# Optimization experiments

Measured on AMD Instinct MI355X. Metric: run time of the kernel, lower is better.

The kernel has to match this reference:

```python
import jax, jax.numpy as jnp
import numpy as np

B, S, F, H = 64, 512, 512, 1024


def setup_inputs() -> dict:
    key = jax.random.key(0)
    ks = jax.random.split(key, 12)
    s_in = 1.0 / np.sqrt(H)
    return {
        "x": jax.random.normal(ks[0], (B, S, F), dtype=jnp.float32),
        "W_ih0": jax.random.uniform(ks[1], (H, F), jnp.float32, -s_in, s_in),
        "W_hh0": jax.random.uniform(ks[2], (H, H), jnp.float32, -s_in, s_in),
        "b_ih0": jax.random.uniform(ks[3], (H,), jnp.float32, -s_in, s_in),
        "b_hh0": jax.random.uniform(ks[4], (H,), jnp.float32, -s_in, s_in),
        "W_ih1": jax.random.uniform(ks[5], (H, H), jnp.float32, -s_in, s_in),
        "W_hh1": jax.random.uniform(ks[6], (H, H), jnp.float32, -s_in, s_in),
        "b_ih1": jax.random.uniform(ks[7], (H,), jnp.float32, -s_in, s_in),
        "b_hh1": jax.random.uniform(ks[8], (H,), jnp.float32, -s_in, s_in),
        "fc_w": jax.random.uniform(ks[9], (1, H), jnp.float32, -s_in, s_in),
        "fc_b": jax.random.uniform(ks[10], (1,), jnp.float32, -s_in, s_in),
    }


def _rnn_layer(x_seq, W_ih, W_hh, b_ih, b_hh):
    # x_seq: [B, S, Fin]; PyTorch RNN step: h_t = tanh(x W_ih^T + b_ih + h W_hh^T + b_hh)
    x_proj = jnp.einsum("bsf,hf->bsh", x_seq, W_ih) + b_ih + b_hh  # precompute input part
    h0 = jnp.zeros((x_seq.shape[0], W_hh.shape[0]), x_seq.dtype)

    def step(h, xp):
        h_new = jnp.tanh(xp + h @ W_hh.T)
        return h_new, h_new

    _, ys = jax.lax.scan(step, h0, jnp.swapaxes(x_proj, 0, 1))  # [S, B, H]
    return jnp.swapaxes(ys, 0, 1)  # [B, S, H]


def reference(x, W_ih0, W_hh0, b_ih0, b_hh0, W_ih1, W_hh1, b_ih1, b_hh1, fc_w, fc_b):
    h1 = _rnn_layer(x, W_ih0, W_hh0, b_ih0, b_hh0)
    h2 = _rnn_layer(h1, W_ih1, W_hh1, b_ih1, b_hh1)
    last = h2[:, -1, :]  # [B, H]
    logits = (last @ fc_w.T + fc_b).squeeze(-1)  # [B]
    return jax.nn.sigmoid(logits)
```

## Files before the change

### kernel.cpp

```cpp
#include <hip/hip_runtime.h>

typedef unsigned short u16;
typedef __attribute__((ext_vector_type(8))) short short8;
typedef __attribute__((ext_vector_type(4))) float f32x4;

#define GLP(p) ((const __attribute__((address_space(1))) void*)(p))
#define LDSP(p) ((__attribute__((address_space(3))) void*)(p))

__device__ inline u16 f2bf(float f) {
  unsigned u = __float_as_uint(f);
  return (u16)((u + 0x7fffu + ((u >> 16) & 1u)) >> 16);
}
__device__ inline float bf2f(u16 h) {
  return __uint_as_float(((unsigned)h) << 16);
}
__device__ inline float tanh_fast(float x) {
  float e = __expf(2.0f * x);
  return 1.0f - 2.0f / (e + 1.0f);
}

__device__ inline void store_short_sc(u16* p, unsigned v) {
  asm volatile("global_store_short %0, %1, off sc0 sc1" :: "v"(p), "v"(v) : "memory");
}
__device__ inline void store_int_sc(int* p, int v) {
  asm volatile("global_store_dword %0, %1, off sc0 sc1" :: "v"(p), "v"(v) : "memory");
}
__device__ inline int load_int_sc(const int* p) {
  int v;
  asm volatile("global_load_dword %0, %1, off sc0 sc1\n\t"
               "s_waitcnt vmcnt(0)"
               : "=&v"(v) : "v"(p) : "memory");
  return v;
}
__device__ inline void load8_sc(const u16* plo, const u16* phi,
                                short8& d0, short8& d1, short8& d2, short8& d3,
                                short8& d4, short8& d5, short8& d6, short8& d7) {
  asm volatile(
      "global_load_dwordx4 %0, %8, off sc0 sc1\n\t"
      "global_load_dwordx4 %1, %8, off offset:1024 sc0 sc1\n\t"
      "global_load_dwordx4 %2, %8, off offset:2048 sc0 sc1\n\t"
      "global_load_dwordx4 %3, %8, off offset:3072 sc0 sc1\n\t"
      "global_load_dwordx4 %4, %9, off sc0 sc1\n\t"
      "global_load_dwordx4 %5, %9, off offset:1024 sc0 sc1\n\t"
      "global_load_dwordx4 %6, %9, off offset:2048 sc0 sc1\n\t"
      "global_load_dwordx4 %7, %9, off offset:3072 sc0 sc1\n\t"
      : "=&v"(d0), "=&v"(d1), "=&v"(d2), "=&v"(d3),
        "=&v"(d4), "=&v"(d5), "=&v"(d6), "=&v"(d7)
      : "v"(plo), "v"(phi)
      : "memory");
}
__device__ inline void wait_all16(short8& a0, short8& a1, short8& a2, short8& a3,
                                  short8& a4, short8& a5, short8& a6, short8& a7,
                                  short8& b0, short8& b1, short8& b2, short8& b3,
                                  short8& b4, short8& b5, short8& b6, short8& b7) {
  asm volatile("s_waitcnt vmcnt(0)"
               : "+v"(a0), "+v"(a1), "+v"(a2), "+v"(a3),
                 "+v"(a4), "+v"(a5), "+v"(a6), "+v"(a7),
                 "+v"(b0), "+v"(b1), "+v"(b2), "+v"(b3),
                 "+v"(b4), "+v"(b5), "+v"(b6), "+v"(b7)
               :: "memory");
}
__device__ inline void poll_flags(const int* fbase, int lane, int target) {
  const int* fp = fbase + lane * 32;
  while (load_int_sc(fp) < target) {}
}

__device__ inline void convseg(const float* __restrict__ s, u16* __restrict__ d,
                               long n4, long t, long S) {
  for (long i = t; i < n4; i += S) {
    float4 v = ((const float4*)s)[i];
    ushort4 o;
    o.x = f2bf(v.x); o.y = f2bf(v.y); o.z = f2bf(v.z); o.w = f2bf(v.w);
    ((ushort4*)d)[i] = o;
  }
}

__global__ __launch_bounds__(256) void prep_kernel(
    const float* __restrict__ x, const float* __restrict__ wih0,
    const float* __restrict__ whh0, const float* __restrict__ wih1,
    const float* __restrict__ whh1,
    u16* __restrict__ xb, u16* __restrict__ wih0b, u16* __restrict__ whh0b,
    u16* __restrict__ wih1b, u16* __restrict__ whh1b,
    u16* __restrict__ hbufs, int* __restrict__ bar) {
  long t = blockIdx.x * 256L + threadIdx.x;
  long S = (long)gridDim.x * 256L;
  convseg(x,    xb,    16777216 / 4, t, S);
  convseg(wih0, wih0b,   524288 / 4, t, S);
  convseg(whh0, whh0b,  1048576 / 4, t, S);
  convseg(wih1, wih1b,  1048576 / 4, t, S);
  convseg(whh1, whh1b,  1048576 / 4, t, S);
  ushort4 z4 = make_ushort4(0, 0, 0, 0);
  for (long i = t; i < 65536; i += S) ((ushort4*)hbufs)[i] = z4;
  int4 zi = make_int4(0, 0, 0, 0);
  for (long i = t; i < 4096; i += S) ((int4*)bar)[i] = zi;
}

__global__ __launch_bounds__(256, 2) void gemm_xproj(
    const u16* __restrict__ A,
    const u16* __restrict__ Bw,
    const float* __restrict__ bi, const float* __restrict__ bh,
    u16* __restrict__ C) {
  __shared__ u16 As[128 * 64];
  __shared__ u16 Bs[128 * 64];
  const int tid = threadIdx.x;
  const int lane = tid & 63;
  const int w = tid >> 6;
  const int ln = lane & 15, kg = lane >> 4;
  const int m0 = blockIdx.x * 128;
  const int n0 = blockIdx.y * 128;
  const int mi = (w & 1) * 64, ni = (w >> 1) * 64;

  f32x4 acc[4][4] = {};
  float bias[4];
#pragma unroll
  for (int nj = 0; nj < 4; ++nj) bias[nj] = bi[n0 + ni + nj * 16 + ln] + bh[n0 + ni + nj * 16 + ln];

  const int lrow = lane >> 3;
  const int lcol = (lane & 7) * 8;

  for (int kt = 0; kt < 512; kt += 64) {
#pragma unroll
    for (int i = 0; i < 4; ++i) {
      int row = i * 32 + w * 8;
      const u16* ga = A + (long)(m0 + row + lrow) * 512 + kt + lcol;
      __builtin_amdgcn_global_load_lds(GLP(ga), LDSP(As + row * 64), 16, 0, 0);
      const u16* gb = Bw + (long)(n0 + row + lrow) * 512 + kt + lcol;
      __builtin_amdgcn_global_load_lds(GLP(gb), LDSP(Bs + row * 64), 16, 0, 0);
    }
    __syncthreads();
#pragma unroll
    for (int kc = 0; kc < 64; kc += 32) {
      short8 af[4], bf[4];
#pragma unroll
      for (int i = 0; i < 4; ++i) {
        af[i] = *(const short8*)(As + (mi + i * 16 + ln) * 64 + kc + kg * 8);
        bf[i] = *(const short8*)(Bs + (ni + i * 16 + ln) * 64 + kc + kg * 8);
      }
#pragma unroll
      for (int a = 0; a < 4; ++a)
#pragma unroll
        for (int b = 0; b < 4; ++b)
          acc[a][b] = __builtin_amdgcn_mfma_f32_16x16x32_bf16(af[a], bf[b], acc[a][b], 0, 0, 0);
    }
    __syncthreads();
  }
#pragma unroll
  for (int a = 0; a < 4; ++a)
#pragma unroll
    for (int b = 0; b < 4; ++b)
#pragma unroll
      for (int r = 0; r < 4; ++r) {
        int m = m0 + mi + a * 16 + kg * 4 + r;
        int n = n0 + ni + b * 16 + ln;
        C[(long)m * 1024 + n] = f2bf(acc[a][b][r] + bias[b]);
      }
}

__global__ __launch_bounds__(256, 1) void rnn_persist(
    const u16* __restrict__ whh0, const u16* __restrict__ wih1,
    const u16* __restrict__ whh1, const u16* __restrict__ xp0,
    const float* __restrict__ bih1, const float* __restrict__ bhh1,
    u16* __restrict__ h1buf, u16* __restrict__ h2buf, int* __restrict__ bar) {
  const int tid = threadIdx.x;
  const int lane = tid & 63;
  const int w = tid >> 6;
  const int ln = lane & 15, kg = lane >> 4;
  const int q = blockIdx.x >> 6;
  const int c = blockIdx.x & 63;
  const int m0 = q * 16;
  const int j0 = c * 16;
  const int kb = w * 256;

  short8 WA[8], W1[8], W2[8];
#pragma unroll
  for (int i = 0; i < 8; ++i) {
    int off = (j0 + ln) * 1024 + kb + i * 32 + kg * 8;
    WA[i] = *(const short8*)(whh0 + off);
    W1[i] = *(const short8*)(wih1 + off);
    W2[i] = *(const short8*)(whh1 + off);
  }
  const float bias1 = bih1[j0 + ln] + bhh1[j0 + ln];

  __shared__ float red[2][2][4][256];
  int* flags = bar + q * 64 * 32;
  int* myF = flags + c * 32;

  const int lbase = (w * 16 + (kg >> 1)) * 256 + ln * 16 + (kg & 1) * 8;
  const u16* hq1 = h1buf + q * 16384 + lbase;
  const u16* hq2 = h2buf + q * 16384 + lbase;

  short8 H1[8], H2[8];
  u16 xpv[4];

  short8 zz = {0, 0, 0, 0, 0, 0, 0, 0};
#pragma unroll
  for (int i = 0; i < 8; ++i) { H1[i] = zz; H2[i] = zz; }
  if (w == 0) {
#pragma unroll
    for (int r = 0; r < 4; ++r)
      xpv[r] = xp0[((long)(m0 + kg * 4 + r) * 512 + 0) * 1024 + j0 + ln];
  }

  for (int it = 0; it <= 512; ++it) {
    const int rp = it & 1;
    f32x4 accA = {}, accB = {};
#pragma unroll
    for (int i = 0; i < 8; ++i) accA = __builtin_amdgcn_mfma_f32_16x16x32_bf16(H1[i], WA[i], accA, 0, 0, 0);
#pragma unroll
    for (int i = 0; i < 8; ++i) accB = __builtin_amdgcn_mfma_f32_16x16x32_bf16(H1[i], W1[i], accB, 0, 0, 0);
#pragma unroll
    for (int i = 0; i < 8; ++i) accB = __builtin_amdgcn_mfma_f32_16x16x32_bf16(H2[i], W2[i], accB, 0, 0, 0);
    *(f32x4*)&red[rp][0][w][lane * 4] = accA;
    *(f32x4*)&red[rp][1][w][lane * 4] = accB;
    __syncthreads();

    if (w == 0) {
      if (it < 512) {
        f32x4 s = *(const f32x4*)&red[rp][0][0][lane * 4];
        s += *(const f32x4*)&red[rp][0][1][lane * 4];
        s += *(const f32x4*)&red[rp][0][2][lane * 4];
        s += *(const f32x4*)&red[rp][0][3][lane * 4];
        u16* h1w = h1buf + (it & 1) * 65536 + q * 16384 + c * 256;
#pragma unroll
        for (int r = 0; r < 4; ++r) {
          float z = s[r] + bf2f(xpv[r]);
          store_short_sc(h1w + (kg * 4 + r) * 16 + ln, (unsigned)f2bf(tanh_fast(z)));
        }
        asm volatile("s_waitcnt vmcnt(0)" ::: "memory");
      }
    } else if (w == 1) {
      if (it >= 1) {
        f32x4 s = *(const f32x4*)&red[rp][1][0][lane * 4];
        s += *(const f32x4*)&red[rp][1][1][lane * 4];
        s += *(const f32x4*)&red[rp][1][2][lane * 4];
        s += *(const f32x4*)&red[rp][1][3][lane * 4];
        u16* h2w = h2buf + ((it + 1) & 1) * 65536 + q * 16384 + c * 256;
#pragma unroll
        for (int r = 0; r < 4; ++r) {
          float z = s[r] + bias1;
          store_short_sc(h2w + (kg * 4 + r) * 16 + ln, (unsigned)f2bf(tanh_fast(z)));
        }
        asm volatile("s_waitcnt vmcnt(0)" ::: "memory");
      }
    }
    __syncthreads();
    if (tid == 0) store_int_sc(myF, it + 1);

    if (it < 512) {
      poll_flags(flags, lane, it + 1);
      const u16* p1 = hq1 + (it & 1) * 65536;
      load8_sc(p1, p1 + 2048, H1[0], H1[1], H1[2], H1[3], H1[4], H1[5], H1[6], H1[7]);
      const u16* p2 = hq2 + ((it + 1) & 1) * 65536;
      load8_sc(p2, p2 + 2048, H2[0], H2[1], H2[2], H2[3], H2[4], H2[5], H2[6], H2[7]);
      if (w == 0 && it < 511) {
#pragma unroll
        for (int r = 0; r < 4; ++r)
          xpv[r] = xp0[((long)(m0 + kg * 4 + r) * 512 + (it + 1)) * 1024 + j0 + ln];
      }
      wait_all16(H1[0], H1[1], H1[2], H1[3], H1[4], H1[5], H1[6], H1[7],
                 H2[0], H2[1], H2[2], H2[3], H2[4], H2[5], H2[6], H2[7]);
    }
  }
}

__global__ __launch_bounds__(256) void fc_kernel(const u16* __restrict__ h2,
                                                 const float* __restrict__ fcw,
                                                 const float* __restrict__ fcb,
                                                 float* __restrict__ out) {
  const int lane = threadIdx.x & 63;
  const int w = threadIdx.x >> 6;
  float wreg[16];
#pragma unroll
  for (int i = 0; i < 16; ++i) wreg[i] = fcw[lane * 16 + i];
  for (int b = w; b < 64; b += 4) {
    const int q = b >> 4, mb = b & 15;
    const u16* hp = h2 + 65536 + q * 16384 + lane * 256 + mb * 16;
    float s = 0.f;
#pragma unroll
    for (int i = 0; i < 16; ++i) s += bf2f(hp[i]) * wreg[i];
#pragma unroll
    for (int off = 32; off > 0; off >>= 1) s += __shfl_down(s, off, 64);
    if (lane == 0) out[b] = 1.0f / (1.0f + __expf(-(s + fcb[0])));
  }
}

extern "C" void kernel_launch(void* const* d_in, const int* in_sizes, int n_in,
                              void* d_out, int out_size, void* d_ws, size_t ws_size,
                              hipStream_t stream) {
  const float* x    = (const float*)d_in[0];
  const float* wih0 = (const float*)d_in[1];
  const float* whh0 = (const float*)d_in[2];
  const float* bih0 = (const float*)d_in[3];
  const float* bhh0 = (const float*)d_in[4];
  const float* wih1 = (const float*)d_in[5];
  const float* whh1 = (const float*)d_in[6];
  const float* bih1 = (const float*)d_in[7];
  const float* bhh1 = (const float*)d_in[8];
  const float* fcw  = (const float*)d_in[9];
  const float* fcb  = (const float*)d_in[10];

  char* ws = (char*)d_ws;
  u16* xb    = (u16*)(ws);
  u16* wih0b = (u16*)(ws + 33554432);
  u16* whh0b = (u16*)(ws + 34603008);
  u16* wih1b = (u16*)(ws + 36700160);
  u16* whh1b = (u16*)(ws + 38797312);
  u16* xp0   = (u16*)(ws + 40894464);
  u16* h1buf = (u16*)(ws + 108003328);
  u16* h2buf = (u16*)(ws + 108265472);
  int* bar   = (int*)(ws + 108527616);

  prep_kernel<<<1024, 256, 0, stream>>>(x, wih0, whh0, wih1, whh1, xb, wih0b,
                                        whh0b, wih1b, whh1b, h1buf, bar);
  dim3 gg(256, 8);
  gemm_xproj<<<gg, 256, 0, stream>>>(xb, wih0b, bih0, bhh0, xp0);
  rnn_persist<<<256, 256, 0, stream>>>(whh0b, wih1b, whh1b, xp0, bih1, bhh1,
                                       h1buf, h2buf, bar);
  fc_kernel<<<1, 256, 0, stream>>>(h2buf, fcw, fcb, (float*)d_out);
}
```

Measured before the change: 1.684 ms.

## Replace post-epilogue block barrier with LDS flag handoff and pipelined flag polling

The second __syncthreads after the tanh epilogue is removed. Wave 0 now waits on an LDS flag set by wave 1 before publishing the cross-block progress flag, so waves 2-3 can go straight to polling. Flag polling keeps two outstanding global loads in flight and uses a wave-wide __all check, which shortens the poll round-trip. This lowers per-timestep synchronization latency in the persistent recurrence, at the cost of more subtle intra-block ordering. The red buffer's double buffering is relied on to keep the epilogue reads safe.

```diff
diff --git a/kernel.cpp b/kernel.cpp
--- a/kernel.cpp
+++ b/kernel.cpp
@@ -24,13 +24,6 @@
 }
 __device__ inline void store_int_sc(int* p, int v) {
   asm volatile("global_store_dword %0, %1, off sc0 sc1" :: "v"(p), "v"(v) : "memory");
-}
-__device__ inline int load_int_sc(const int* p) {
-  int v;
-  asm volatile("global_load_dword %0, %1, off sc0 sc1\n\t"
-               "s_waitcnt vmcnt(0)"
-               : "=&v"(v) : "v"(p) : "memory");
-  return v;
 }
 __device__ inline void load8_sc(const u16* plo, const u16* phi,
                                 short8& d0, short8& d1, short8& d2, short8& d3,
@@ -60,9 +53,20 @@
                  "+v"(b4), "+v"(b5), "+v"(b6), "+v"(b7)
                :: "memory");
 }
-__device__ inline void poll_flags(const int* fbase, int lane, int target) {
-  const int* fp = fbase + lane * 32;
-  while (load_int_sc(fp) < target) {}
+__device__ inline void poll_flags_pipe(const int* fp, int target) {
+  int r0, r1;
+  asm volatile(
+      "global_load_dword %0, %2, off sc0 sc1\n\t"
+      "global_load_dword %1, %2, off sc0 sc1"
+      : "=&v"(r0), "=&v"(r1) : "v"(fp) : "memory");
+  while (true) {
+    asm volatile("s_waitcnt vmcnt(1)" : "+v"(r0) :: "memory");
+    if (__all(r0 >= target)) break;
+    asm volatile("global_load_dword %0, %1, off sc0 sc1" : "=&v"(r0) : "v"(fp) : "memory");
+    asm volatile("s_waitcnt vmcnt(1)" : "+v"(r1) :: "memory");
+    if (__all(r1 >= target)) break;
+    asm volatile("global_load_dword %0, %1, off sc0 sc1" : "=&v"(r1) : "v"(fp) : "memory");
+  }
 }
 
 __device__ inline void convseg(const float* __restrict__ s, u16* __restrict__ d,
@@ -182,8 +186,10 @@
   const float bias1 = bih1[j0 + ln] + bhh1[j0 + ln];
 
   __shared__ float red[2][2][4][256];
+  __shared__ int done2;
   int* flags = bar + q * 64 * 32;
   int* myF = flags + c * 32;
+  const int* pF = flags + lane * 32;
 
   const int lbase = (w * 16 + (kg >> 1)) * 256 + ln * 16 + (kg & 1) * 8;
   const u16* hq1 = h1buf + q * 16384 + lbase;
@@ -192,6 +198,8 @@
   short8 H1[8], H2[8];
   u16 xpv[4];
 
+  if (tid == 0) done2 = 0;
+
   short8 zz = {0, 0, 0, 0, 0, 0, 0, 0};
 #pragma unroll
   for (int i = 0; i < 8; ++i) { H1[i] = zz; H2[i] = zz; }
@@ -200,6 +208,7 @@
     for (int r = 0; r < 4; ++r)
       xpv[r] = xp0[((long)(m0 + kg * 4 + r) * 512 + 0) * 1024 + j0 + ln];
   }
+  __syncthreads();
 
   for (int it = 0; it <= 512; ++it) {
     const int rp = it & 1;
@@ -227,6 +236,9 @@
           store_short_sc(h1w + (kg * 4 + r) * 16 + ln, (unsigned)f2bf(tanh_fast(z)));
         }
         asm volatile("s_waitcnt vmcnt(0)" ::: "memory");
+        while (__hip_atomic_load(&done2, __ATOMIC_ACQUIRE,
+                                 __HIP_MEMORY_SCOPE_WORKGROUP) < it + 1) {}
+        if (lane == 0) store_int_sc(myF, it + 1);
       }
     } else if (w == 1) {
       if (it >= 1) {
@@ -242,12 +254,13 @@
         }
         asm volatile("s_waitcnt vmcnt(0)" ::: "memory");
       }
+      if (lane == 0)
+        __hip_atomic_store(&done2, it + 1, __ATOMIC_RELEASE,
+                           __HIP_MEMORY_SCOPE_WORKGROUP);
     }
-    __syncthreads();
-    if (tid == 0) store_int_sc(myF, it + 1);
 
     if (it < 512) {
-      poll_flags(flags, lane, it + 1);
+      poll_flags_pipe(pF, it + 1);
       const u16* p1 = hq1 + (it & 1) * 65536;
       load8_sc(p1, p1 + 2048, H1[0], H1[1], H1[2], H1[3], H1[4], H1[5], H1[6], H1[7]);
       const u16* p2 = hq2 + ((it + 1) & 1) * 65536;
```

Result: slower. 2.412 ms (+43.3%).

## Fuse layer-0 input projection into persistent RNN kernel, drop xproj GEMM

Applied to the files above, without the earlier changes.

Removes the separate gemm_xproj kernel and its large bf16 xp0 intermediate. Each persistent block now keeps its slice of W_ih0 in registers, loads the per-step x slice alongside the hidden-state loads, and adds four extra MFMAs per step to compute the input projection inline. The bias is added as a scalar. This saves the GEMM launch and the write and read of the projection buffer. In exchange, the latency-bound recurrent loop does more loads and MFMAs per step and uses more registers.

```diff
diff --git a/kernel.cpp b/kernel.cpp
--- a/kernel.cpp
+++ b/kernel.cpp
@@ -49,15 +49,29 @@
       : "v"(plo), "v"(phi)
       : "memory");
 }
-__device__ inline void wait_all16(short8& a0, short8& a1, short8& a2, short8& a3,
+__device__ inline void load4_x(const u16* p0, const u16* p1,
+                               const u16* p2, const u16* p3,
+                               short8& x0, short8& x1, short8& x2, short8& x3) {
+  asm volatile(
+      "global_load_dwordx4 %0, %4, off\n\t"
+      "global_load_dwordx4 %1, %5, off\n\t"
+      "global_load_dwordx4 %2, %6, off\n\t"
+      "global_load_dwordx4 %3, %7, off"
+      : "=&v"(x0), "=&v"(x1), "=&v"(x2), "=&v"(x3)
+      : "v"(p0), "v"(p1), "v"(p2), "v"(p3)
+      : "memory");
+}
+__device__ inline void wait_all20(short8& a0, short8& a1, short8& a2, short8& a3,
                                   short8& a4, short8& a5, short8& a6, short8& a7,
                                   short8& b0, short8& b1, short8& b2, short8& b3,
-                                  short8& b4, short8& b5, short8& b6, short8& b7) {
+                                  short8& b4, short8& b5, short8& b6, short8& b7,
+                                  short8& x0, short8& x1, short8& x2, short8& x3) {
   asm volatile("s_waitcnt vmcnt(0)"
                : "+v"(a0), "+v"(a1), "+v"(a2), "+v"(a3),
                  "+v"(a4), "+v"(a5), "+v"(a6), "+v"(a7),
                  "+v"(b0), "+v"(b1), "+v"(b2), "+v"(b3),
-                 "+v"(b4), "+v"(b5), "+v"(b6), "+v"(b7)
+                 "+v"(b4), "+v"(b5), "+v"(b6), "+v"(b7),
+                 "+v"(x0), "+v"(x1), "+v"(x2), "+v"(x3)
                :: "memory");
 }
 __device__ inline void poll_flags(const int* fbase, int lane, int target) {
@@ -95,70 +109,11 @@
   for (long i = t; i < 4096; i += S) ((int4*)bar)[i] = zi;
 }
 
-__global__ __launch_bounds__(256, 2) void gemm_xproj(
-    const u16* __restrict__ A,
-    const u16* __restrict__ Bw,
-    const float* __restrict__ bi, const float* __restrict__ bh,
-    u16* __restrict__ C) {
-  __shared__ u16 As[128 * 64];
-  __shared__ u16 Bs[128 * 64];
-  const int tid = threadIdx.x;
-  const int lane = tid & 63;
-  const int w = tid >> 6;
-  const int ln = lane & 15, kg = lane >> 4;
-  const int m0 = blockIdx.x * 128;
-  const int n0 = blockIdx.y * 128;
-  const int mi = (w & 1) * 64, ni = (w >> 1) * 64;
-
-  f32x4 acc[4][4] = {};
-  float bias[4];
-#pragma unroll
-  for (int nj = 0; nj < 4; ++nj) bias[nj] = bi[n0 + ni + nj * 16 + ln] + bh[n0 + ni + nj * 16 + ln];
-
-  const int lrow = lane >> 3;
-  const int lcol = (lane & 7) * 8;
-
-  for (int kt = 0; kt < 512; kt += 64) {
-#pragma unroll
-    for (int i = 0; i < 4; ++i) {
-      int row = i * 32 + w * 8;
-      const u16* ga = A + (long)(m0 + row + lrow) * 512 + kt + lcol;
-      __builtin_amdgcn_global_load_lds(GLP(ga), LDSP(As + row * 64), 16, 0, 0);
-      const u16* gb = Bw + (long)(n0 + row + lrow) * 512 + kt + lcol;
-      __builtin_amdgcn_global_load_lds(GLP(gb), LDSP(Bs + row * 64), 16, 0, 0);
-    }
-    __syncthreads();
-#pragma unroll
-    for (int kc = 0; kc < 64; kc += 32) {
-      short8 af[4], bf[4];
-#pragma unroll
-      for (int i = 0; i < 4; ++i) {
-        af[i] = *(const short8*)(As + (mi + i * 16 + ln) * 64 + kc + kg * 8);
-        bf[i] = *(const short8*)(Bs + (ni + i * 16 + ln) * 64 + kc + kg * 8);
-      }
-#pragma unroll
-      for (int a = 0; a < 4; ++a)
-#pragma unroll
-        for (int b = 0; b < 4; ++b)
-          acc[a][b] = __builtin_amdgcn_mfma_f32_16x16x32_bf16(af[a], bf[b], acc[a][b], 0, 0, 0);
-    }
-    __syncthreads();
-  }
-#pragma unroll
-  for (int a = 0; a < 4; ++a)
-#pragma unroll
-    for (int b = 0; b < 4; ++b)
-#pragma unroll
-      for (int r = 0; r < 4; ++r) {
-        int m = m0 + mi + a * 16 + kg * 4 + r;
-        int n = n0 + ni + b * 16 + ln;
-        C[(long)m * 1024 + n] = f2bf(acc[a][b][r] + bias[b]);
-      }
-}
-
 __global__ __launch_bounds__(256, 1) void rnn_persist(
-    const u16* __restrict__ whh0, const u16* __restrict__ wih1,
-    const u16* __restrict__ whh1, const u16* __restrict__ xp0,
+    const u16* __restrict__ wih0, const u16* __restrict__ whh0,
+    const u16* __restrict__ wih1, const u16* __restrict__ whh1,
+    const u16* __restrict__ xb,
+    const float* __restrict__ bih0, const float* __restrict__ bhh0,
     const float* __restrict__ bih1, const float* __restrict__ bhh1,
     u16* __restrict__ h1buf, u16* __restrict__ h2buf, int* __restrict__ bar) {
   const int tid = threadIdx.x;
@@ -170,8 +125,9 @@
   const int m0 = q * 16;
   const int j0 = c * 16;
   const int kb = w * 256;
-
-  short8 WA[8], W1[8], W2[8];
+  const int fb = w * 128;
+
+  short8 WA[8], W1[8], W2[8], WI[4];
 #pragma unroll
   for (int i = 0; i < 8; ++i) {
     int off = (j0 + ln) * 1024 + kb + i * 32 + kg * 8;
@@ -179,6 +135,10 @@
     W1[i] = *(const short8*)(wih1 + off);
     W2[i] = *(const short8*)(whh1 + off);
   }
+#pragma unroll
+  for (int i = 0; i < 4; ++i)
+    WI[i] = *(const short8*)(wih0 + (j0 + ln) * 512 + fb + i * 32 + kg * 8);
+  const float bias0 = bih0[j0 + ln] + bhh0[j0 + ln];
   const float bias1 = bih1[j0 + ln] + bhh1[j0 + ln];
 
   __shared__ float red[2][2][4][256];
@@ -188,22 +148,21 @@
   const int lbase = (w * 16 + (kg >> 1)) * 256 + ln * 16 + (kg & 1) * 8;
   const u16* hq1 = h1buf + q * 16384 + lbase;
   const u16* hq2 = h2buf + q * 16384 + lbase;
-
-  short8 H1[8], H2[8];
-  u16 xpv[4];
+  const u16* xrow = xb + (long)(m0 + ln) * 262144 + fb + kg * 8;
+
+  short8 H1[8], H2[8], X[4];
 
   short8 zz = {0, 0, 0, 0, 0, 0, 0, 0};
 #pragma unroll
   for (int i = 0; i < 8; ++i) { H1[i] = zz; H2[i] = zz; }
-  if (w == 0) {
-#pragma unroll
-    for (int r = 0; r < 4; ++r)
-      xpv[r] = xp0[((long)(m0 + kg * 4 + r) * 512 + 0) * 1024 + j0 + ln];
-  }
+#pragma unroll
+  for (int i = 0; i < 4; ++i) X[i] = *(const short8*)(xrow + i * 32);
 
   for (int it = 0; it <= 512; ++it) {
     const int rp = it & 1;
     f32x4 accA = {}, accB = {};
+#pragma unroll
+    for (int i = 0; i < 4; ++i) accA = __builtin_amdgcn_mfma_f32_16x16x32_bf16(X[i], WI[i], accA, 0, 0, 0);
 #pragma unroll
     for (int i = 0; i < 8; ++i) accA = __builtin_amdgcn_mfma_f32_16x16x32_bf16(H1[i], WA[i], accA, 0, 0, 0);
 #pragma unroll
@@ -223,7 +182,7 @@
         u16* h1w = h1buf + (it & 1) * 65536 + q * 16384 + c * 256;
 #pragma unroll
         for (int r = 0; r < 4; ++r) {
-          float z = s[r] + bf2f(xpv[r]);
+          float z = s[r] + bias0;
           store_short_sc(h1w + (kg * 4 + r) * 16 + ln, (unsigned)f2bf(tanh_fast(z)));
         }
         asm volatile("s_waitcnt vmcnt(0)" ::: "memory");
@@ -252,13 +211,13 @@
       load8_sc(p1, p1 + 2048, H1[0], H1[1], H1[2], H1[3], H1[4], H1[5], H1[6], H1[7]);
       const u16* p2 = hq2 + ((it + 1) & 1) * 65536;
       load8_sc(p2, p2 + 2048, H2[0], H2[1], H2[2], H2[3], H2[4], H2[5], H2[6], H2[7]);
-      if (w == 0 && it < 511) {
-#pragma unroll
-        for (int r = 0; r < 4; ++r)
-          xpv[r] = xp0[((long)(m0 + kg * 4 + r) * 512 + (it + 1)) * 1024 + j0 + ln];
+      if (it < 511) {
+        const u16* xr = xrow + (long)(it + 1) * 512;
+        load4_x(xr, xr + 32, xr + 64, xr + 96, X[0], X[1], X[2], X[3]);
       }
-      wait_all16(H1[0], H1[1], H1[2], H1[3], H1[4], H1[5], H1[6], H1[7],
-                 H2[0], H2[1], H2[2], H2[3], H2[4], H2[5], H2[6], H2[7]);
+      wait_all20(H1[0], H1[1], H1[2], H1[3], H1[4], H1[5], H1[6], H1[7],
+                 H2[0], H2[1], H2[2], H2[3], H2[4], H2[5], H2[6], H2[7],
+                 X[0], X[1], X[2], X[3]);
     }
   }
 }
@@ -305,16 +264,14 @@
   u16* whh0b = (u16*)(ws + 34603008);
   u16* wih1b = (u16*)(ws + 36700160);
   u16* whh1b = (u16*)(ws + 38797312);
-  u16* xp0   = (u16*)(ws + 40894464);
   u16* h1buf = (u16*)(ws + 108003328);
   u16* h2buf = (u16*)(ws + 108265472);
   int* bar   = (int*)(ws + 108527616);
 
   prep_kernel<<<1024, 256, 0, stream>>>(x, wih0, whh0, wih1, whh1, xb, wih0b,
                                         whh0b, wih1b, whh1b, h1buf, bar);
-  dim3 gg(256, 8);
-  gemm_xproj<<<gg, 256, 0, stream>>>(xb, wih0b, bih0, bhh0, xp0);
-  rnn_persist<<<256, 256, 0, stream>>>(whh0b, wih1b, whh1b, xp0, bih1, bhh1,
+  rnn_persist<<<256, 256, 0, stream>>>(wih0b, whh0b, wih1b, whh1b, xb,
+                                       bih0, bhh0, bih1, bhh1,
                                        h1buf, h2buf, bar);
   fc_kernel<<<1, 256, 0, stream>>>(h2buf, fcw, fcb, (float*)d_out);
 }
```

New measurement: 1.855 ms. +10.2%, slower.
